# Performance work log

Measured on AMD Instinct MI355X. Metric: run time of the kernel, lower is better.

## Reference

```python
import jax, jax.numpy as jnp
import numpy as np

ROT_DIM = 32  # min(32, dim_head)

def rotate_half(t):
    # '... (j d) -> ... j d' with j=2, unbind, cat(-x2, x1)
    x1, x2 = jnp.split(t, 2, axis=-1)
    return jnp.concatenate((-x2, x1), axis=-1)

def apply_rotary(pos, t):
    rot_dim = pos.shape[-1]
    t_rot, t_pass = t[..., :rot_dim], t[..., rot_dim:]
    t_rot = t_rot * jnp.cos(pos) + rotate_half(t_rot) * jnp.sin(pos)
    return jnp.concatenate((t_rot, t_pass), axis=-1)

def setup_inputs() -> dict:
    key = jax.random.key(0)
    k1, k2, k3 = jax.random.split(key, 3)
    b, n, dim = 2, 2048, 2048
    inner = 16 * 128
    x = jax.random.normal(k1, (b, n, dim), dtype=jnp.float32)
    w_qkv = jax.random.normal(k2, (3 * inner, dim), dtype=jnp.float32) * (dim ** -0.5)
    w_out = jax.random.normal(k3, (inner, dim), dtype=jnp.float32) * (inner ** -0.5)
    g = jnp.ones((dim,), dtype=jnp.float32)
    return {"x": x, "w_qkv": w_qkv, "w_out": w_out, "g": g}

def reference(x, w_qkv, w_out, g):
    b, n, dim = x.shape
    h, d = 16, 128
    scale = d ** -0.5
    # NOTE: original code computes qkv from RAW x; the LayerNorm result is unused.
    qkv = jnp.einsum('bnc,fc->bnf', x, w_qkv)  # [b, n, 3*h*d]
    q, k, v = jnp.split(qkv, 3, axis=-1)
    def to_heads(t):  # b n (h d) -> (b h) n d
        return t.reshape(b, n, h, d).transpose(0, 2, 1, 3).reshape(b * h, n, d)
    q, k, v = map(to_heads, (q, k, v))
    # rotary positions: freqs [n, ROT_DIM//2], cat -> [n, ROT_DIM]
    inv_freq = 1.0 / (10000.0 ** (jnp.arange(0, ROT_DIM, 2, dtype=jnp.float32) / ROT_DIM))
    freqs = jnp.arange(n, dtype=jnp.float32)[:, None] * inv_freq[None, :]
    pos = jnp.concatenate((freqs, freqs), axis=-1)  # [n, ROT_DIM]
    q = apply_rotary(pos, q)
    k = apply_rotary(pos, k)
    q = q * scale
    sim = jnp.einsum('bid,bjd->bij', q, k)  # [(b h), n, n]
    causal_mask = jnp.triu(jnp.ones((n, n), dtype=bool), 1)
    neg = -jnp.finfo(sim.dtype).max
    sim = jnp.where(causal_mask[None], neg, sim)
    attn = jax.nn.softmax(sim, axis=-1)
    out = jnp.einsum('bij,bjd->bid', attn, v)  # [(b h), n, d]
    out = out.reshape(b, h, n, d).transpose(0, 2, 1, 3).reshape(b, n, h * d)
    return jnp.einsum('bnf,fc->bnc', out, w_out.T)  # Linear(inner, dim): y = out @ w_out^T with w_out [inner, dim]? see note
```

## Files before the change

kernel.cpp:

```cpp
#include <hip/hip_runtime.h>
#include <hip/hip_bf16.h>
#include <stdint.h>

typedef __bf16 bf16_t;
typedef __bf16 bf16x8 __attribute__((ext_vector_type(8)));
typedef float  f32x4  __attribute__((ext_vector_type(4)));

__device__ __forceinline__ void gload16(const void* gp, void* lp) {
  __builtin_amdgcn_global_load_lds(
      (const __attribute__((address_space(1))) void*)(uintptr_t)gp,
      (__attribute__((address_space(3))) void*)(uintptr_t)lp,
      16, 0, 0);
}

__device__ __forceinline__ f32x4 mfma16(bf16x8 a, bf16x8 b, f32x4 c) {
  return __builtin_amdgcn_mfma_f32_16x16x32_bf16(a, b, c, 0, 0, 0);
}

__device__ __forceinline__ uint32_t pack2(float a, float b) {
  uint16_t ba = __builtin_bit_cast(uint16_t, (bf16_t)a);
  uint16_t bb = __builtin_bit_cast(uint16_t, (bf16_t)b);
  return (uint32_t)ba | ((uint32_t)bb << 16);
}

__global__ __launch_bounds__(256) void cast_all(const float* __restrict__ x,
                                                const float* __restrict__ wqkv,
                                                const float* __restrict__ wout,
                                                bf16_t* __restrict__ xb,
                                                bf16_t* __restrict__ wqkvb,
                                                bf16_t* __restrict__ woutb) {
  const int N1 = 1048576, N2 = 1572864, N3 = 524288;
  int i = blockIdx.x * 256 + threadIdx.x;
  int stride = gridDim.x * 256;
  for (; i < N1 + N2 + N3; i += stride) {
    const float* in; bf16_t* out; int j;
    if (i < N1)           { in = x;    out = xb;    j = i; }
    else if (i < N1 + N2) { in = wqkv; out = wqkvb; j = i - N1; }
    else                  { in = wout; out = woutb; j = i - N1 - N2; }
    const f32x4* p = (const f32x4*)in + (size_t)j * 2;
    f32x4 a = p[0], b = p[1];
    bf16x8 o;
    o[0] = (bf16_t)a[0]; o[1] = (bf16_t)a[1]; o[2] = (bf16_t)a[2]; o[3] = (bf16_t)a[3];
    o[4] = (bf16_t)b[0]; o[5] = (bf16_t)b[1]; o[6] = (bf16_t)b[2]; o[7] = (bf16_t)b[3];
    ((bf16x8*)out)[j] = o;
  }
}

__global__ __launch_bounds__(512, 2) void gemm_qkv(const bf16_t* __restrict__ A,
                                                   const bf16_t* __restrict__ B,
                                                   bf16_t* __restrict__ C,
                                                   int M, int N, int K) {
  __shared__ __align__(16) bf16_t As[2][256 * 32];
  __shared__ __align__(16) bf16_t Bs[2][384 * 32];
  const int t = threadIdx.x;
  const int wid = t >> 6, l = t & 63;
  const int l15 = l & 15, l4 = l >> 4;
  const int wm = wid >> 2, wn = wid & 3;
  const long m0 = (long)blockIdx.x * 256;
  const long n0 = (long)blockIdx.y * 384;
  const int KT = K >> 5;

  auto stageA = [&](int kt, bf16_t* __restrict__ LB) {
    #pragma unroll
    for (int it = 0; it < 2; ++it) {
      int s = it * 512 + t;
      int r = s >> 2, c = s & 3;
      int cs = c ^ ((r >> 1) & 3);
      gload16(A + (m0 + r) * (long)K + kt * 32 + cs * 8, LB + r * 32 + c * 8);
    }
  };
  auto stageB = [&](int kt, bf16_t* __restrict__ LB) {
    #pragma unroll
    for (int it = 0; it < 3; ++it) {
      int s = it * 512 + t;
      int r = s >> 2, c = s & 3;
      int cs = c ^ ((r >> 1) & 3);
      gload16(B + (n0 + r) * (long)K + kt * 32 + cs * 8, LB + r * 32 + c * 8);
    }
  };
  auto ldfrag = [&](const bf16_t* buf, int rloc) -> bf16x8 {
    int cs = l4 ^ ((rloc >> 1) & 3);
    return *(const bf16x8*)(buf + rloc * 32 + cs * 8);
  };

  f32x4 acc[8][6] = {};

  stageB(0, &Bs[0][0]);
  stageA(0, &As[0][0]);
  stageB(1, &Bs[1][0]);
  asm volatile("s_waitcnt vmcnt(3)" ::: "memory");
  asm volatile("s_barrier" ::: "memory");

  for (int kt = 0; kt < KT; ++kt) {
    const bf16_t* Ab = &As[kt & 1][0];
    const bf16_t* Bb = &Bs[kt & 1][0];
    const bool stA = (kt + 1 < KT), stB = (kt + 2 < KT);

    bf16x8 bfr[6];
    #pragma unroll
    for (int nr = 0; nr < 6; ++nr) bfr[nr] = ldfrag(Bb, wn * 96 + nr * 16 + l15);
    {
      bf16x8 a0 = ldfrag(Ab, wm * 128 + 0 * 16 + l15);
      bf16x8 a1 = ldfrag(Ab, wm * 128 + 1 * 16 + l15);
      bf16x8 a2 = ldfrag(Ab, wm * 128 + 2 * 16 + l15);
      bf16x8 a3 = ldfrag(Ab, wm * 128 + 3 * 16 + l15);
      if (stA) stageA(kt + 1, &As[(kt + 1) & 1][0]);
      asm volatile("s_barrier" ::: "memory");
      __builtin_amdgcn_s_setprio(1);
      #pragma unroll
      for (int nr = 0; nr < 6; ++nr) {
        acc[0][nr] = mfma16(a0, bfr[nr], acc[0][nr]);
        acc[1][nr] = mfma16(a1, bfr[nr], acc[1][nr]);
        acc[2][nr] = mfma16(a2, bfr[nr], acc[2][nr]);
        acc[3][nr] = mfma16(a3, bfr[nr], acc[3][nr]);
      }
      __builtin_amdgcn_s_setprio(0);
      asm volatile("s_barrier" ::: "memory");
    }
    {
      bf16x8 a4 = ldfrag(Ab, wm * 128 + 4 * 16 + l15);
      bf16x8 a5 = ldfrag(Ab, wm * 128 + 5 * 16 + l15);
      bf16x8 a6 = ldfrag(Ab, wm * 128 + 6 * 16 + l15);
      bf16x8 a7 = ldfrag(Ab, wm * 128 + 7 * 16 + l15);
      if (stB) stageB(kt + 2, &Bs[kt & 1][0]);
      asm volatile("s_barrier" ::: "memory");
      __builtin_amdgcn_s_setprio(1);
      #pragma unroll
      for (int nr = 0; nr < 6; ++nr) {
        acc[4][nr] = mfma16(a4, bfr[nr], acc[4][nr]);
        acc[5][nr] = mfma16(a5, bfr[nr], acc[5][nr]);
        acc[6][nr] = mfma16(a6, bfr[nr], acc[6][nr]);
        acc[7][nr] = mfma16(a7, bfr[nr], acc[7][nr]);
      }
      __builtin_amdgcn_s_setprio(0);
      if (stB) asm volatile("s_waitcnt vmcnt(3)" ::: "memory");
      else     asm volatile("s_waitcnt vmcnt(0)" ::: "memory");
      asm volatile("s_barrier" ::: "memory");
    }
  }

  const int nrA = ((128 - ((wn * 96) & 127)) & 127) >> 4;
  const float L2D16 = 0.8304820237218406f;
  const float invf = exp2f(-(float)l15 * L2D16);
  const float qscale = 0.08838834764831845f;
  const float INV2PI = 0.15915494309189535f;
  const float TWOPI  = 6.283185307179586f;
  const bool doRot = (nrA < 6) && ((n0 + wn * 96 + nrA * 16) < 4096);
  #pragma unroll
  for (int mr = 0; mr < 8; ++mr) {
    const long r0 = m0 + wm * 128 + mr * 16 + l4 * 4;
    if (doRot) {
      float sv[4], cv[4];
      #pragma unroll
      for (int i = 0; i < 4; ++i) {
        float ang = (float)((int)(r0 + i) & 2047) * invf;
        float rev = ang * INV2PI;
        rev -= floorf(rev);
        float r2 = rev * TWOPI;
        sv[i] = __sinf(r2);
        cv[i] = __cosf(r2);
      }
      #pragma unroll
      for (int nr = 0; nr < 5; ++nr) {
        if (nr == nrA) {
          #pragma unroll
          for (int i = 0; i < 4; ++i) {
            float a = acc[mr][nr][i], b2 = acc[mr][nr + 1][i];
            acc[mr][nr][i]     = a * cv[i] - b2 * sv[i];
            acc[mr][nr + 1][i] = b2 * cv[i] + a * sv[i];
          }
        }
      }
    }
    #pragma unroll
    for (int nr = 0; nr < 6; ++nr) {
      const long f0 = n0 + wn * 96 + nr * 16;
      if (f0 < 2048) {
        #pragma unroll
        for (int i = 0; i < 4; ++i) acc[mr][nr][i] *= qscale;
      }
      #pragma unroll
      for (int i = 0; i < 4; ++i)
        C[(r0 + i) * N + f0 + l15] = (bf16_t)acc[mr][nr][i];
    }
  }
}

template<bool OUT_BF16>
__global__ __launch_bounds__(512, 2) void gemm8p_bt(const bf16_t* __restrict__ A,
                                                    const bf16_t* __restrict__ B,
                                                    void* __restrict__ Cout,
                                                    int M, int N, int K) {
  __shared__ __align__(16) bf16_t As[2][128 * 64];
  __shared__ __align__(16) bf16_t Bs[2][256 * 64];
  const int t = threadIdx.x;
  const int wid = t >> 6, l = t & 63;
  const int l15 = l & 15, l4 = l >> 4;
  const int wm = wid >> 2, wn = wid & 3;
  const long m0 = (long)blockIdx.x * 128;
  const long n0 = (long)blockIdx.y * 256;
  const int KT = K >> 6;

  auto stageA = [&](int kt, bf16_t* __restrict__ LB) {
    #pragma unroll
    for (int it = 0; it < 2; ++it) {
      int s = it * 512 + t;
      int r = s >> 3, c = s & 7;
      gload16(A + (m0 + r) * (long)K + kt * 64 + ((c ^ (r & 7)) << 3),
              LB + r * 64 + c * 8);
    }
  };
  auto stageB = [&](int kt, bf16_t* __restrict__ LB) {
    #pragma unroll
    for (int it = 0; it < 4; ++it) {
      int s = it * 512 + t;
      int r = s >> 3, c = s & 7;
      gload16(B + (n0 + r) * (long)K + kt * 64 + ((c ^ (r & 7)) << 3),
              LB + r * 64 + c * 8);
    }
  };
  auto ldfrag = [&](const bf16_t* buf, int rloc, int kk) -> bf16x8 {
    return *(const bf16x8*)(buf + rloc * 64 + ((((kk << 2) + l4) ^ (rloc & 7)) << 3));
  };

  f32x4 acc[4][4] = {};

  stageB(0, &Bs[0][0]);
  stageA(0, &As[0][0]);
  stageB(1, &Bs[1][0]);
  asm volatile("s_waitcnt vmcnt(4)" ::: "memory");
  asm volatile("s_barrier" ::: "memory");

  for (int kt = 0; kt < KT; ++kt) {
    const bf16_t* Ab = &As[kt & 1][0];
    const bf16_t* Bb = &Bs[kt & 1][0];
    const bool stA = (kt + 1 < KT), stB = (kt + 2 < KT);

    bf16x8 bfr[4][2];
    #pragma unroll
    for (int nr = 0; nr < 4; ++nr)
      #pragma unroll
      for (int kk = 0; kk < 2; ++kk)
        bfr[nr][kk] = ldfrag(Bb, wn * 64 + nr * 16 + l15, kk);
    {
      bf16x8 a00 = ldfrag(Ab, wm * 64 + 0 * 16 + l15, 0);
      bf16x8 a01 = ldfrag(Ab, wm * 64 + 0 * 16 + l15, 1);
      bf16x8 a10 = ldfrag(Ab, wm * 64 + 1 * 16 + l15, 0);
      bf16x8 a11 = ldfrag(Ab, wm * 64 + 1 * 16 + l15, 1);
      if (stA) stageA(kt + 1, &As[(kt + 1) & 1][0]);
      asm volatile("s_barrier" ::: "memory");
      __builtin_amdgcn_s_setprio(1);
      #pragma unroll
      for (int nr = 0; nr < 4; ++nr) {
        acc[0][nr] = mfma16(a00, bfr[nr][0], acc[0][nr]);
        acc[0][nr] = mfma16(a01, bfr[nr][1], acc[0][nr]);
        acc[1][nr] = mfma16(a10, bfr[nr][0], acc[1][nr]);
        acc[1][nr] = mfma16(a11, bfr[nr][1], acc[1][nr]);
      }
      __builtin_amdgcn_s_setprio(0);
      asm volatile("s_barrier" ::: "memory");
    }
    {
      bf16x8 a00 = ldfrag(Ab, wm * 64 + 2 * 16 + l15, 0);
      bf16x8 a01 = ldfrag(Ab, wm * 64 + 2 * 16 + l15, 1);
      bf16x8 a10 = ldfrag(Ab, wm * 64 + 3 * 16 + l15, 0);
      bf16x8 a11 = ldfrag(Ab, wm * 64 + 3 * 16 + l15, 1);
      if (stB) stageB(kt + 2, &Bs[kt & 1][0]);
      asm volatile("s_barrier" ::: "memory");
      __builtin_amdgcn_s_setprio(1);
      #pragma unroll
      for (int nr = 0; nr < 4; ++nr) {
        acc[2][nr] = mfma16(a00, bfr[nr][0], acc[2][nr]);
        acc[2][nr] = mfma16(a01, bfr[nr][1], acc[2][nr]);
        acc[3][nr] = mfma16(a10, bfr[nr][0], acc[3][nr]);
        acc[3][nr] = mfma16(a11, bfr[nr][1], acc[3][nr]);
      }
      __builtin_amdgcn_s_setprio(0);
      if (stB) asm volatile("s_waitcnt vmcnt(4)" ::: "memory");
      else     asm volatile("s_waitcnt vmcnt(0)" ::: "memory");
      asm volatile("s_barrier" ::: "memory");
    }
  }

  #pragma unroll
  for (int mr = 0; mr < 4; ++mr)
    #pragma unroll
    for (int nr = 0; nr < 4; ++nr)
      #pragma unroll
      for (int i = 0; i < 4; ++i) {
        long r = m0 + wm * 64 + mr * 16 + l4 * 4 + i;
        long c = n0 + wn * 64 + nr * 16 + l15;
        if (OUT_BF16) ((bf16_t*)Cout)[r * N + c] = (bf16_t)acc[mr][nr][i];
        else          ((float*)Cout)[r * N + c] = acc[mr][nr][i];
      }
}

__global__ __launch_bounds__(512, 4) void attn_causal(const bf16_t* __restrict__ qkv,
                                                      bf16_t* __restrict__ ao) {
  const int id = blockIdx.x;
  const int qt = (id < 256) ? (15 - (id >> 5)) : ((id - 256) >> 5);
  const int bh = id & 31;
  const int b = bh >> 4, h = bh & 15;
  const int t = threadIdx.x;
  const int wid = t >> 6, l = t & 63;
  const int l15 = l & 15, l4 = l >> 4;
  __shared__ __align__(16) bf16_t Ks0[64 * 128];
  __shared__ __align__(16) bf16_t Ks1[64 * 128];
  __shared__ __align__(16) bf16_t Vt[2][128 * 64];
  __shared__ __align__(16) bf16_t Pb[8][16 * 64];
  const bf16_t* base = qkv + (long)b * 2048 * 6144 + h * 128;
  const int q0w = qt * 128 + wid * 16;
  bf16x8 qf[4];
  #pragma unroll
  for (int ks = 0; ks < 4; ++ks)
    qf[ks] = *(const bf16x8*)(base + (long)(q0w + l15) * 6144 + ks * 32 + l4 * 8);
  f32x4 o[8] = {};
  float mrun = -1.0e30f, lrun = 0.f;
  bf16_t* pbuf = Pb[wid];
  bf16x8 vr0, vr1;
  const int ntiles = 2 * qt + 2;

  auto stageK = [&](int tile, bf16_t* dst) {
    const bf16_t* src = base + 2048 + (long)tile * 64 * 6144;
    #pragma unroll
    for (int it = 0; it < 2; ++it) {
      int s = it * 512 + t;
      int krow = s >> 4, kc = s & 15;
      int ksc = kc ^ (krow & 7);
      gload16(src + (long)krow * 6144 + ksc * 8, dst + (size_t)s * 8);
    }
  };
  auto loadV = [&](int tile) {
    const bf16_t* vsr = base + 4096 + (long)(tile * 64 + l) * 6144;
    vr0 = *(const bf16x8*)(vsr + wid * 8);
    vr1 = *(const bf16x8*)(vsr + (8 + wid) * 8);
  };
  auto writeVt = [&](bf16_t* vt) {
    #pragma unroll
    for (int it = 0; it < 2; ++it) {
      int c = it * 8 + wid;
      bf16x8 v = it ? vr1 : vr0;
      #pragma unroll
      for (int e = 0; e < 8; ++e) {
        int d = c * 8 + e;
        vt[d * 64 + (((l >> 3) ^ e) * 8) + (l & 7)] = v[e];
      }
    }
  };
  auto compute = [&](int kv0, const bf16_t* ksb, const bf16_t* vt) {
    if (kv0 > q0w + 15) return;
    f32x4 sa[4] = {};
    __builtin_amdgcn_s_setprio(1);
    #pragma unroll
    for (int ks = 0; ks < 4; ++ks) {
      #pragma unroll
      for (int nb = 0; nb < 4; ++nb) {
        int row = nb * 16 + l15;
        int cs = (ks * 4 + l4) ^ (row & 7);
        bf16x8 kf = *(const bf16x8*)(ksb + row * 128 + cs * 8);
        sa[nb] = mfma16(kf, qf[ks], sa[nb]);
      }
    }
    __builtin_amdgcn_s_setprio(0);
    if (kv0 + 63 > q0w) {
      const int q = q0w + l15;
      #pragma unroll
      for (int nb = 0; nb < 4; ++nb)
        #pragma unroll
        for (int i = 0; i < 4; ++i)
          if (kv0 + nb * 16 + l4 * 4 + i > q) sa[nb][i] = -3.0e38f;
    }
    f32x4 mv;
    #pragma unroll
    for (int i = 0; i < 4; ++i)
      mv[i] = fmaxf(fmaxf(sa[0][i], sa[1][i]), fmaxf(sa[2][i], sa[3][i]));
    float pmax = fmaxf(fmaxf(mv[0], mv[1]), fmaxf(mv[2], mv[3]));
    pmax = fmaxf(pmax, __shfl_xor(pmax, 16));
    pmax = fmaxf(pmax, __shfl_xor(pmax, 32));
    if (!__all(pmax - mrun <= 8.0f)) {
      float mnew = fmaxf(mrun, pmax);
      float corr = __expf(mrun - mnew);
      mrun = mnew;
      lrun *= corr;
      float cc[4];
      #pragma unroll
      for (int i = 0; i < 4; ++i) cc[i] = __shfl(corr, l4 * 4 + i);
      #pragma unroll
      for (int nf = 0; nf < 8; ++nf)
        #pragma unroll
        for (int i = 0; i < 4; ++i) o[nf][i] *= cc[i];
    }
    float ps = 0.f;
    #pragma unroll
    for (int nb = 0; nb < 4; ++nb)
      #pragma unroll
      for (int i = 0; i < 4; ++i) {
        float p = __expf(sa[nb][i] - mrun);
        sa[nb][i] = p;
        ps += p;
      }
    ps += __shfl_xor(ps, 16);
    ps += __shfl_xor(ps, 32);
    lrun += ps;
    #pragma unroll
    for (int nb = 0; nb < 4; ++nb) {
      int cw = (nb * 2 + (l4 >> 1)) ^ (l15 & 7);
      uint32_t* dst = (uint32_t*)(pbuf + l15 * 64 + cw * 8 + (l4 & 1) * 4);
      dst[0] = pack2(sa[nb][0], sa[nb][1]);
      dst[1] = pack2(sa[nb][2], sa[nb][3]);
    }
    #pragma unroll
    for (int ks2 = 0; ks2 < 2; ++ks2) {
      bf16x8 pf = *(const bf16x8*)(pbuf + l15 * 64 + (((ks2 * 4 + l4) ^ (l15 & 7)) * 8));
      __builtin_amdgcn_s_setprio(1);
      #pragma unroll
      for (int nf = 0; nf < 8; ++nf) {
        int row = nf * 16 + l15;
        bf16x8 vf = *(const bf16x8*)(vt + row * 64 + (((ks2 * 4 + l4) ^ (row & 7)) * 8));
        o[nf] = mfma16(pf, vf, o[nf]);
      }
      __builtin_amdgcn_s_setprio(0);
    }
  };

  stageK(0, Ks0);
  loadV(0);
  writeVt(Vt[0]);
  __syncthreads();
  for (int tile = 0; tile < ntiles; ++tile) {
    bf16_t* curK = (tile & 1) ? Ks1 : Ks0;
    bf16_t* nxtK = (tile & 1) ? Ks0 : Ks1;
    bf16_t* curV = Vt[tile & 1];
    bf16_t* nxtV = Vt[(tile + 1) & 1];
    const bool pre = (tile + 1 < ntiles);
    if (pre) { stageK(tile + 1, nxtK); loadV(tile + 1); }
    compute(tile * 64, curK, curV);
    if (pre) writeVt(nxtV);
    __syncthreads();
  }
  float linv = 1.f / lrun;
  float li[4];
  #pragma unroll
  for (int i = 0; i < 4; ++i) li[i] = __shfl(linv, l4 * 4 + i);
  bf16_t* aob = ao + (long)b * 2048 * 2048 + h * 128;
  #pragma unroll
  for (int i = 0; i < 4; ++i) {
    long qrow = q0w + l4 * 4 + i;
    #pragma unroll
    for (int nf = 0; nf < 8; ++nf)
      aob[qrow * 2048 + nf * 16 + l15] = (bf16_t)(o[nf][i] * li[i]);
  }
}

extern "C" void kernel_launch(void* const* d_in, const int* in_sizes, int n_in,
                              void* d_out, int out_size, void* d_ws, size_t ws_size,
                              hipStream_t stream) {
  const float* x     = (const float*)d_in[0];
  const float* w_qkv = (const float*)d_in[1];
  const float* w_out = (const float*)d_in[2];
  char* ws = (char*)d_ws;
  bf16_t* xb    = (bf16_t*)(ws + 0L);
  bf16_t* wqkvb = (bf16_t*)(ws + 16777216L);
  bf16_t* woutb = (bf16_t*)(ws + 41943040L);
  bf16_t* qkv   = (bf16_t*)(ws + 50331648L);
  bf16_t* ao    = (bf16_t*)(ws + 100663296L);

  cast_all<<<2048, 256, 0, stream>>>(x, w_qkv, w_out, xb, wqkvb, woutb);
  gemm_qkv<<<dim3(16, 16), 512, 0, stream>>>(xb, wqkvb, qkv, 4096, 6144, 2048);
  attn_causal<<<512, 512, 0, stream>>>(qkv, ao);
  gemm8p_bt<false><<<dim3(32, 8), 512, 0, stream>>>(ao, woutb, d_out, 4096, 2048, 2048);
}
```

Baseline: 222.9 us.

## Triple-buffer K tiles and double-buffer V registers in causal attention

The attention kernel now prefetches K two tiles ahead through a three-slot LDS ring, and alternates two register sets for V so that its global load runs a full tile ahead. The loop is unrolled by two, and each __syncthreads is replaced by an explicit s_waitcnt vmcnt(4) plus s_barrier, so the newest loads can stay in flight across the barrier. Launch bounds drop from 4 to 2 waves-per-EU to leave room for the extra registers and LDS, which lowers occupancy. The block-to-query-tile mapping becomes a plain descending order instead of the split ordering.

```diff
diff --git a/kernel.cpp b/kernel.cpp
--- a/kernel.cpp
+++ b/kernel.cpp
@@ -295,17 +295,16 @@
       }
 }
 
-__global__ __launch_bounds__(512, 4) void attn_causal(const bf16_t* __restrict__ qkv,
+__global__ __launch_bounds__(512, 2) void attn_causal(const bf16_t* __restrict__ qkv,
                                                       bf16_t* __restrict__ ao) {
   const int id = blockIdx.x;
-  const int qt = (id < 256) ? (15 - (id >> 5)) : ((id - 256) >> 5);
+  const int qt = 15 - (id >> 5);
   const int bh = id & 31;
   const int b = bh >> 4, h = bh & 15;
   const int t = threadIdx.x;
   const int wid = t >> 6, l = t & 63;
   const int l15 = l & 15, l4 = l >> 4;
-  __shared__ __align__(16) bf16_t Ks0[64 * 128];
-  __shared__ __align__(16) bf16_t Ks1[64 * 128];
+  __shared__ __align__(16) bf16_t Ks[3][64 * 128];
   __shared__ __align__(16) bf16_t Vt[2][128 * 64];
   __shared__ __align__(16) bf16_t Pb[8][16 * 64];
   const bf16_t* base = qkv + (long)b * 2048 * 6144 + h * 128;
@@ -317,10 +316,10 @@
   f32x4 o[8] = {};
   float mrun = -1.0e30f, lrun = 0.f;
   bf16_t* pbuf = Pb[wid];
-  bf16x8 vr0, vr1;
   const int ntiles = 2 * qt + 2;
 
-  auto stageK = [&](int tile, bf16_t* dst) {
+  auto stageK = [&](int tile) {
+    bf16_t* dst = Ks[tile % 3];
     const bf16_t* src = base + 2048 + (long)tile * 64 * 6144;
     #pragma unroll
     for (int it = 0; it < 2; ++it) {
@@ -330,16 +329,16 @@
       gload16(src + (long)krow * 6144 + ksc * 8, dst + (size_t)s * 8);
     }
   };
-  auto loadV = [&](int tile) {
+  auto loadV = [&](int tile, bf16x8& v0, bf16x8& v1) {
     const bf16_t* vsr = base + 4096 + (long)(tile * 64 + l) * 6144;
-    vr0 = *(const bf16x8*)(vsr + wid * 8);
-    vr1 = *(const bf16x8*)(vsr + (8 + wid) * 8);
-  };
-  auto writeVt = [&](bf16_t* vt) {
+    v0 = *(const bf16x8*)(vsr + wid * 8);
+    v1 = *(const bf16x8*)(vsr + (8 + wid) * 8);
+  };
+  auto writeVt = [&](bf16_t* vt, const bf16x8& v0, const bf16x8& v1) {
     #pragma unroll
     for (int it = 0; it < 2; ++it) {
       int c = it * 8 + wid;
-      bf16x8 v = it ? vr1 : vr0;
+      bf16x8 v = it ? v1 : v0;
       #pragma unroll
       for (int e = 0; e < 8; ++e) {
         int d = c * 8 + e;
@@ -423,20 +422,32 @@
     }
   };
 
-  stageK(0, Ks0);
-  loadV(0);
-  writeVt(Vt[0]);
-  __syncthreads();
-  for (int tile = 0; tile < ntiles; ++tile) {
-    bf16_t* curK = (tile & 1) ? Ks1 : Ks0;
-    bf16_t* nxtK = (tile & 1) ? Ks0 : Ks1;
-    bf16_t* curV = Vt[tile & 1];
-    bf16_t* nxtV = Vt[(tile + 1) & 1];
-    const bool pre = (tile + 1 < ntiles);
-    if (pre) { stageK(tile + 1, nxtK); loadV(tile + 1); }
-    compute(tile * 64, curK, curV);
-    if (pre) writeVt(nxtV);
-    __syncthreads();
+  bf16x8 vA0, vA1, vB0, vB1;
+  stageK(0);
+  stageK(1);
+  loadV(0, vA0, vA1);
+  writeVt(Vt[0], vA0, vA1);
+  if (ntiles > 1) loadV(1, vB0, vB1);
+  asm volatile("s_waitcnt vmcnt(0) lgkmcnt(0)" ::: "memory");
+  asm volatile("s_barrier" ::: "memory");
+
+  for (int tt = 0; tt < ntiles; tt += 2) {
+    {
+      const bool p2 = (tt + 2 < ntiles);
+      if (p2) { loadV(tt + 2, vA0, vA1); stageK(tt + 2); }
+      compute(tt * 64, Ks[tt % 3], Vt[0]);
+      if (tt + 1 < ntiles) writeVt(Vt[1], vB0, vB1);
+      asm volatile("s_waitcnt vmcnt(4) lgkmcnt(0)" ::: "memory");
+      asm volatile("s_barrier" ::: "memory");
+    }
+    if (tt + 1 < ntiles) {
+      const bool p2 = (tt + 3 < ntiles);
+      if (p2) { loadV(tt + 3, vB0, vB1); stageK(tt + 3); }
+      compute((tt + 1) * 64, Ks[(tt + 1) % 3], Vt[1]);
+      if (tt + 2 < ntiles) writeVt(Vt[0], vA0, vA1);
+      asm volatile("s_waitcnt vmcnt(4) lgkmcnt(0)" ::: "memory");
+      asm volatile("s_barrier" ::: "memory");
+    }
   }
   float linv = 1.f / lrun;
   float li[4];
```

New measurement: 227.3 us. No clear change (+1.9%).
